# Kernel optimization log

Hardware: AMD Instinct MI355X
Metric: run time of the kernel (lower is better)

The kernel has to match this reference:

```python
import jax, jax.numpy as jnp
from jax import lax
import numpy as np

DN = ('NHWC', 'HWIO', 'NHWC')  # NHWC activations, HWIO kernels (TF layout)
EPS = 1e-3


def setup_inputs() -> dict:
    key = jax.random.key(0)
    ks = jax.random.split(key, 6)
    B, H, W, C = 16, 64, 64, 256
    x = jax.random.normal(ks[0], (B, H, W, C), jnp.float32)
    # per-sample predicted kernels (scaled to keep activations well-conditioned)
    depthwise_kernels = jax.random.normal(ks[1], (B, 3, 3, C, C), jnp.float32) * 0.02
    pointwise_kernels = jax.random.normal(ks[2], (B, 1, 1, C, C), jnp.float32) * 0.06
    biases = jax.random.normal(ks[3], (B, C), jnp.float32) * 0.1
    # shared trailing Conv2D layer params
    conv_w = jax.random.normal(ks[4], (3, 3, C, C), jnp.float32) * 0.02
    conv_b = jnp.zeros((C,), jnp.float32)
    return dict(x=x, depthwise_kernels=depthwise_kernels,
                pointwise_kernels=pointwise_kernels, biases=biases,
                conv_w=conv_w, conv_b=conv_b)


def _instance_norm(x):
    # tf.nn.moments over spatial dims (population variance), eps=0.001
    mean = jnp.mean(x, axis=(1, 2), keepdims=True)
    var = jnp.var(x, axis=(1, 2), keepdims=True)
    return (x - mean) * lax.rsqrt(var + EPS)


def _reflect_pad_hw(x, p=1):
    pad = [(0, 0)] * (x.ndim - 3) + [(p, p), (p, p), (0, 0)]
    return jnp.pad(x, pad, mode='reflect')


def _per_sample_conv(xi, dk, pk, bi):
    # xi: [H,W,C]; dk: [3,3,C,Cm]; pk: [1,1,Cm,Co]; bi: [Co]
    xp = _reflect_pad_hw(xi)[None]  # [1,H+2,W+2,C]
    y = lax.conv_general_dilated(xp, dk, (1, 1), 'VALID', dimension_numbers=DN)
    y = lax.conv_general_dilated(y, pk, (1, 1), 'VALID', dimension_numbers=DN)
    return (y + bi)[0]


def reference(x, depthwise_kernels, pointwise_kernels, biases, conv_w, conv_b):
    x = _instance_norm(x)
    # per-sample kernels -> vmap over batch (replaces tf.map_fn)
    x = jax.vmap(_per_sample_conv)(x, depthwise_kernels, pointwise_kernels, biases)
    # shared Conv2D: reflect pad + VALID conv + bias
    xp = _reflect_pad_hw(x)
    y = lax.conv_general_dilated(xp, conv_w, (1, 1), 'VALID', dimension_numbers=DN)
    return y + conv_b
```

## Files before the change

### kernel.cpp

```cpp
#include <hip/hip_runtime.h>


typedef __bf16 bf16x8 __attribute__((ext_vector_type(8)));
typedef float f32x4 __attribute__((ext_vector_type(4)));

__device__ __forceinline__ float bf2f(unsigned short v) {
    return __uint_as_float(((unsigned int)v) << 16);
}
__device__ __forceinline__ unsigned short f2bf(float f) {
    unsigned int u = __float_as_uint(f);
    unsigned int r = (u + 0x7FFFu + ((u >> 16) & 1u)) >> 16;
    return (unsigned short)r;
}
__device__ __forceinline__ float ldg_elem(const void* p, size_t idx, bool isbf) {
    return isbf ? bf2f(((const unsigned short*)p)[idx]) : ((const float*)p)[idx];
}

__device__ __forceinline__ void gload16(const void* g, void* l) {
    __builtin_amdgcn_global_load_lds(
        (__attribute__((address_space(1))) void*)(unsigned long long)g,
        (__attribute__((address_space(3))) void*)(unsigned long long)l,
        16, 0, 0);
}

#define RAW_BARRIER() do { asm volatile("" ::: "memory"); \
                           __builtin_amdgcn_s_barrier();   \
                           asm volatile("" ::: "memory"); } while (0)

__global__ void detect_dtype(const unsigned short* __restrict__ x, int* __restrict__ flag) {
    __shared__ int wild;
    if (threadIdx.x == 0) wild = 0;
    __syncthreads();
    int cnt = 0;
    for (int i = 0; i < 16; ++i) {
        float a = fabsf(bf2f(x[threadIdx.x * 16 + i]));
        if (!(a < 64.f) || (a != 0.f && a < 1e-5f)) cnt++;
    }
    atomicAdd(&wild, cnt);
    __syncthreads();
    if (threadIdx.x == 0) *flag = (wild > 512) ? 0 : 1;
}


__global__ void init_stats(float* s) { s[blockIdx.x * 256 + threadIdx.x] = 0.f; }

__global__ void norm_partial(const void* __restrict__ x, const int* __restrict__ flag,
                             float* __restrict__ ssum, float* __restrict__ ssq) {
    const bool isbf = (*flag != 0);
    const int b = blockIdx.x, chunk = blockIdx.y, c = threadIdx.x;
    const size_t base = ((size_t)(b * 4096 + chunk * 64)) * 256 + c;
    float s = 0.f, q = 0.f;
    for (int i = 0; i < 64; ++i) {
        float v = ldg_elem(x, base + (size_t)i * 256, isbf);
        s += v; q += v * v;
    }
    atomicAdd(&ssum[b * 256 + c], s);
    atomicAdd(&ssq[b * 256 + c], q);
}

__global__ void norm_finalize(float* ssum, float* ssq) {
    int i = blockIdx.x * 256 + threadIdx.x;
    float mean = ssum[i] * (1.f / 4096.f);
    float var  = ssq[i]  * (1.f / 4096.f) - mean * mean;
    ssum[i] = mean;
    ssq[i]  = rsqrtf(var + 1e-3f);
}

__global__ void norm_apply(const void* __restrict__ x, const int* __restrict__ flag,
                           const float* __restrict__ mean, const float* __restrict__ rstd,
                           unsigned short* __restrict__ xn) {
    const bool isbf = (*flag != 0);
    size_t e = ((size_t)blockIdx.x * 256 + threadIdx.x) * 8;
    int c0 = (int)(e & 255);
    int bc = (int)(e >> 20) * 256 + c0;
    float v[8];
    if (isbf) {
        uint4 raw = *(const uint4*)((const unsigned short*)x + e);
        unsigned int rr[4] = {raw.x, raw.y, raw.z, raw.w};
#pragma unroll
        for (int i = 0; i < 4; ++i) {
            v[2 * i]     = bf2f((unsigned short)(rr[i] & 0xFFFF));
            v[2 * i + 1] = bf2f((unsigned short)(rr[i] >> 16));
        }
    } else {
        float4 f0 = *(const float4*)((const float*)x + e);
        float4 f1 = *(const float4*)((const float*)x + e + 4);
        v[0] = f0.x; v[1] = f0.y; v[2] = f0.z; v[3] = f0.w;
        v[4] = f1.x; v[5] = f1.y; v[6] = f1.z; v[7] = f1.w;
    }
    unsigned int o[4];
#pragma unroll
    for (int i = 0; i < 4; ++i) {
        unsigned short lo = f2bf((v[2 * i]     - mean[bc + 2 * i])     * rstd[bc + 2 * i]);
        unsigned short hi = f2bf((v[2 * i + 1] - mean[bc + 2 * i + 1]) * rstd[bc + 2 * i + 1]);
        o[i] = (unsigned int)lo | ((unsigned int)hi << 16);
    }
    uint4 out; out.x = o[0]; out.y = o[1]; out.z = o[2]; out.w = o[3];
    *(uint4*)(xn + e) = out;
}

template <bool SCALE>
__global__ void transpose_wk(const void* __restrict__ src, const int* __restrict__ flag,
                             unsigned short* __restrict__ dst,
                             int s_per, long dstBStride, int coStride,
                             const float* __restrict__ rstd) {
    __shared__ unsigned short tile[64][66];
    const bool isbf = (*flag != 0);
    const int sl = blockIdx.x;
    const int b = sl / s_per;
    const size_t dbase = (size_t)b * (size_t)dstBStride + (size_t)(sl % s_per) * 256;
    const int ci0 = blockIdx.y * 64, co0 = blockIdx.z * 64;
    const int t = threadIdx.x;
    const int co4 = (t & 15) * 4;
    const int r0 = t >> 4;
#pragma unroll
    for (int i = 0; i < 4; ++i) {
        int r = r0 + i * 16;
        size_t sidx = (size_t)sl * 65536 + (size_t)(ci0 + r) * 256 + co0 + co4;
        if (isbf) {
            ushort4 v = *(const ushort4*)((const unsigned short*)src + sidx);
            tile[r][co4] = v.x; tile[r][co4 + 1] = v.y;
            tile[r][co4 + 2] = v.z; tile[r][co4 + 3] = v.w;
        } else {
            float4 v = *(const float4*)((const float*)src + sidx);
            tile[r][co4] = f2bf(v.x); tile[r][co4 + 1] = f2bf(v.y);
            tile[r][co4 + 2] = f2bf(v.z); tile[r][co4 + 3] = f2bf(v.w);
        }
    }
    __syncthreads();
    const int cip = (t & 31) * 2;
    const int cob = t >> 5;
    float s0 = 1.f, s1 = 1.f;
    if (SCALE) { s0 = rstd[b * 256 + ci0 + cip]; s1 = rstd[b * 256 + ci0 + cip + 1]; }
#pragma unroll
    for (int i = 0; i < 8; ++i) {
        int co = cob + i * 8;
        unsigned short lo = tile[cip][co], hi = tile[cip + 1][co];
        if (SCALE) { lo = f2bf(bf2f(lo) * s0); hi = f2bf(bf2f(hi) * s1); }
        *(unsigned int*)(dst + dbase + (size_t)(co0 + co) * coStride + ci0 + cip) =
            (unsigned int)lo | ((unsigned int)hi << 16);
    }
}

__global__ void corr_kernel(const unsigned short* __restrict__ dkT,
                            const float* __restrict__ mean,
                            float* __restrict__ negcorr) {
    const int b = blockIdx.x;
    const int lane = threadIdx.x & 63;
    const int co = blockIdx.y * 4 + (threadIdx.x >> 6);
    const unsigned short* wp = dkT + (size_t)(b * 256 + co) * 2304;
    const float* mb = mean + b * 256;
    const int ci0 = (lane & 31) * 8;
    float4 ma = *(const float4*)(mb + ci0);
    float4 mc = *(const float4*)(mb + ci0 + 4);
    float mm[8] = {ma.x, ma.y, ma.z, ma.w, mc.x, mc.y, mc.z, mc.w};
    float sum = 0.f;
#pragma unroll
    for (int c = 0; c < 5; ++c) {
        int k = c * 512 + lane * 8;
        if (k < 2304) {
            uint4 w = *(const uint4*)(wp + k);
            unsigned int wsv[4] = {w.x, w.y, w.z, w.w};
#pragma unroll
            for (int j = 0; j < 4; ++j) {
                sum += bf2f((unsigned short)(wsv[j] & 0xFFFF)) * mm[2 * j];
                sum += bf2f((unsigned short)(wsv[j] >> 16)) * mm[2 * j + 1];
            }
        }
    }
#pragma unroll
    for (int off = 32; off > 0; off >>= 1) sum += __shfl_down(sum, off);
    if (lane == 0) negcorr[b * 256 + co] = -sum;
}

template <int KSLICES, bool PER_SAMPLE_W, int BIAS_MODE, bool IS3X3, bool OUT_F32>
__global__ __launch_bounds__(512, 2) void gemm_conv_256(const unsigned short* __restrict__ src,
                                                        const int* __restrict__ flag,
                                                        const unsigned short* __restrict__ wT,
                                                        const void* __restrict__ bias,
                                                        void* __restrict__ dst) {
    constexpr int KTOT = KSLICES * 256;
    constexpr int NKT = KTOT / 64;
    static_assert(NKT >= 2, "pipeline needs >=2 K-tiles");
    extern __shared__ unsigned short smem[];

    const int t = threadIdx.x;
    const int lane = t & 63;
    const int wave = t >> 6;
    const int wr = wave >> 2;
    const int wc = wave & 3;
    const int b = blockIdx.z;
    const int m0 = blockIdx.x * 256;
    const unsigned short* srcB = src + (size_t)b * (4096 * 256);
    const unsigned short* wB = wT + (PER_SAMPLE_W ? (size_t)b * 256 * KTOT : (size_t)0);
    const bool in_bf = (BIAS_MODE >= 2) ? (*flag != 0) : true;

    const int trow = t >> 3;
    const int tswz = ((t & 7) ^ (trow & 7)) << 3;
    int hU[4], wU[4];
#pragma unroll
    for (int u = 0; u < 4; ++u) {
        int m = m0 + u * 64 + trow;
        hU[u] = m >> 6; wU[u] = m & 63;
    }
    const unsigned short* gBu[4];
#pragma unroll
    for (int u = 0; u < 4; ++u)
        gBu[u] = wB + (size_t)(u * 64 + trow) * KTOT + tswz;

    f32x4 acc[8][4];
#pragma unroll
    for (int i = 0; i < 8; ++i)
#pragma unroll
        for (int j = 0; j < 4; ++j) acc[i][j] = (f32x4){0.f, 0.f, 0.f, 0.f};

    const int fr = lane & 15;
    const int quad = lane >> 4;
    const int fsw = fr & 7;
    const int ks0 = ((quad) ^ fsw) << 3;
    const int ks1 = ((quad + 4) ^ fsw) << 3;
    const int rm = wr * 128;
    const int cn = wc * 64;

#pragma unroll
    for (int kt = 0; kt < 2; ++kt) {
        const int s0_ = kt >> 2;
        const int pdh = IS3X3 ? (s0_ / 3) - 1 : 0;
        const int pdw = IS3X3 ? (s0_ % 3) - 1 : 0;
        const int pchb = (kt & 3) << 6;
        unsigned short* ldsAW = smem + kt * 32768 + wave * 512;
#pragma unroll
        for (int u = 0; u < 4; ++u) {
            int hh = hU[u] + pdh; hh = (hh < 0) ? 1 : (hh > 63 ? 62 : hh);
            int ww = wU[u] + pdw; ww = (ww < 0) ? 1 : (ww > 63 ? 62 : ww);
            gload16(srcB + (size_t)((hh << 6) + ww) * 256 + pchb + tswz, ldsAW + u * 4096);
        }
#pragma unroll
        for (int u = 0; u < 4; ++u)
            gload16(gBu[u] + (size_t)kt * 64, ldsAW + 16384 + u * 4096);
    }
    asm volatile("s_waitcnt vmcnt(8)" ::: "memory");
    RAW_BARRIER();

    bf16x8 af[4][2], bfr[4][2];

    for (int i = 0; i < NKT; ++i) {
        const int buf = i & 1;
        const unsigned short* As_b = smem + buf * 32768;
        const unsigned short* Bs_b = As_b + 16384;
        unsigned short* ldsAW = smem + buf * 32768 + wave * 512;
        const int kt2 = i + 2;
        const bool st = (kt2 < NKT);
        int dh2 = 0, dw2 = 0, chb2 = 0;
        if (st) {
            int s2 = kt2 >> 2;
            dh2 = IS3X3 ? (s2 / 3) - 1 : 0;
            dw2 = IS3X3 ? (s2 % 3) - 1 : 0;
            chb2 = (kt2 & 3) << 6;
        }

#pragma unroll
        for (int m = 0; m < 4; ++m) {
            const unsigned short* rp = As_b + (rm + m * 16 + fr) * 64;
            af[m][0] = *(const bf16x8*)(rp + ks0);
            af[m][1] = *(const bf16x8*)(rp + ks1);
        }
#pragma unroll
        for (int n = 0; n < 2; ++n) {
            const unsigned short* rp = Bs_b + (cn + n * 16 + fr) * 64;
            bfr[n][0] = *(const bf16x8*)(rp + ks0);
            bfr[n][1] = *(const bf16x8*)(rp + ks1);
        }
        __builtin_amdgcn_s_setprio(1);
#pragma unroll
        for (int m = 0; m < 4; ++m)
#pragma unroll
            for (int n = 0; n < 2; ++n) {
                acc[m][n] = __builtin_amdgcn_mfma_f32_16x16x32_bf16(af[m][0], bfr[n][0], acc[m][n], 0, 0, 0);
                acc[m][n] = __builtin_amdgcn_mfma_f32_16x16x32_bf16(af[m][1], bfr[n][1], acc[m][n], 0, 0, 0);
            }
        __builtin_amdgcn_s_setprio(0);

#pragma unroll
        for (int n = 2; n < 4; ++n) {
            const unsigned short* rp = Bs_b + (cn + n * 16 + fr) * 64;
            bfr[n][0] = *(const bf16x8*)(rp + ks0);
            bfr[n][1] = *(const bf16x8*)(rp + ks1);
        }
        __builtin_amdgcn_s_setprio(1);
#pragma unroll
        for (int m = 0; m < 4; ++m)
#pragma unroll
            for (int n = 2; n < 4; ++n) {
                acc[m][n] = __builtin_amdgcn_mfma_f32_16x16x32_bf16(af[m][0], bfr[n][0], acc[m][n], 0, 0, 0);
                acc[m][n] = __builtin_amdgcn_mfma_f32_16x16x32_bf16(af[m][1], bfr[n][1], acc[m][n], 0, 0, 0);
            }
        __builtin_amdgcn_s_setprio(0);

#pragma unroll
        for (int m = 0; m < 4; ++m) {
            const unsigned short* rp = As_b + (rm + 64 + m * 16 + fr) * 64;
            af[m][0] = *(const bf16x8*)(rp + ks0);
            af[m][1] = *(const bf16x8*)(rp + ks1);
        }
        __builtin_amdgcn_s_setprio(1);
#pragma unroll
        for (int m = 0; m < 4; ++m)
#pragma unroll
            for (int n = 0; n < 4; ++n) {
                acc[4 + m][n] = __builtin_amdgcn_mfma_f32_16x16x32_bf16(af[m][0], bfr[n][0], acc[4 + m][n], 0, 0, 0);
                acc[4 + m][n] = __builtin_amdgcn_mfma_f32_16x16x32_bf16(af[m][1], bfr[n][1], acc[4 + m][n], 0, 0, 0);
            }
        __builtin_amdgcn_s_setprio(0);

        RAW_BARRIER();
        if (st) {
#pragma unroll
            for (int u = 0; u < 4; ++u) {
                int hh = hU[u] + dh2; hh = (hh < 0) ? 1 : (hh > 63 ? 62 : hh);
                int ww = wU[u] + dw2; ww = (ww < 0) ? 1 : (ww > 63 ? 62 : ww);
                gload16(srcB + (size_t)((hh << 6) + ww) * 256 + chb2 + tswz, ldsAW + u * 4096);
            }
#pragma unroll
            for (int u = 0; u < 4; ++u)
                gload16(gBu[u] + (size_t)kt2 * 64, ldsAW + 16384 + u * 4096);
            asm volatile("s_waitcnt vmcnt(8)" ::: "memory");
        } else if (i + 1 < NKT) {
            asm volatile("s_waitcnt vmcnt(0)" ::: "memory");
        }
        RAW_BARRIER();
    }

    const int rbase = quad * 4;
    float bv[4];
#pragma unroll
    for (int n = 0; n < 4; ++n) {
        int nn = cn + n * 16 + fr;
        if (BIAS_MODE == 2)      bv[n] = ldg_elem(bias, b * 256 + nn, in_bf);
        else if (BIAS_MODE == 3) bv[n] = ldg_elem(bias, nn, in_bf);
        else                     bv[n] = 0.f;
    }
#pragma unroll
    for (int m = 0; m < 8; ++m) {
#pragma unroll
        for (int rr = 0; rr < 4; ++rr) {
            int mm = m0 + rm + m * 16 + rbase + rr;
            size_t rowoff = ((size_t)b * 4096 + mm) * 256;
#pragma unroll
            for (int n = 0; n < 4; ++n) {
                int nn = cn + n * 16 + fr;
                float val = acc[m][n][rr] + bv[n];
                if (OUT_F32) ((float*)dst)[rowoff + nn] = val;
                else         ((unsigned short*)dst)[rowoff + nn] = f2bf(val);
            }
        }
    }
}

template <int KSLICES, bool PER_SAMPLE_W, int BIAS_MODE, bool IS3X3, bool OUT_F32>
__global__ __launch_bounds__(256) void gemm_conv_dma(const unsigned short* __restrict__ src,
                                                     const int* __restrict__ flag,
                                                     const unsigned short* __restrict__ wT,
                                                     const void* __restrict__ bias,
                                                     void* __restrict__ dst) {
    constexpr int KTOT = KSLICES * 256;
    __shared__ unsigned short As[128 * 64];
    __shared__ unsigned short Bs[128 * 64];

    const int t = threadIdx.x;
    const int lane = t & 63;
    const int wave = t >> 6;
    const int b = blockIdx.z;
    const int m0 = blockIdx.x * 128;
    const int n0 = blockIdx.y * 128;
    const unsigned short* srcB = src + (size_t)b * (4096 * 256);
    const unsigned short* wB = wT + (PER_SAMPLE_W ? (size_t)b * 256 * KTOT : (size_t)0);
    const bool in_bf = (BIAS_MODE >= 2) ? (*flag != 0) : true;

    f32x4 acc[4][4];
#pragma unroll
    for (int i = 0; i < 4; ++i)
#pragma unroll
        for (int j = 0; j < 4; ++j) acc[i][j] = (f32x4){0.f, 0.f, 0.f, 0.f};

    const int lr = lane >> 3;
    const int cidx = lane & 7;
    const int swz = ((cidx ^ lr) << 3);

    int hA[4], wA[4];
    const unsigned short* gB[4];
    unsigned short* ldsA[4];
    unsigned short* ldsB[4];
#pragma unroll
    for (int c = 0; c < 4; ++c) {
        int r = wave * 32 + c * 8;
        int m = m0 + r + lr;
        hA[c] = m >> 6; wA[c] = m & 63;
        gB[c] = wB + (size_t)(n0 + r + lr) * KTOT + swz;
        ldsA[c] = As + r * 64;
        ldsB[c] = Bs + r * 64;
    }

    const int fr = lane & 15;
    const int quad = lane >> 4;
    const int rm = (wave >> 1) * 64;
    const int cn = (wave & 1) * 64;
    const int fsw = fr & 7;

    for (int s = 0; s < KSLICES; ++s) {
        const int dh = IS3X3 ? (s / 3) - 1 : 0;
        const int dw = IS3X3 ? (s % 3) - 1 : 0;
        const unsigned short* gA[4];
#pragma unroll
        for (int c = 0; c < 4; ++c) {
            int hh = hA[c] + dh; hh = (hh < 0) ? 1 : (hh > 63 ? 62 : hh);
            int ww = wA[c] + dw; ww = (ww < 0) ? 1 : (ww > 63 ? 62 : ww);
            gA[c] = srcB + (size_t)((hh << 6) + ww) * 256 + swz;
        }
        const int kbase = s * 256;
#pragma unroll
        for (int cc = 0; cc < 4; ++cc) {
            __syncthreads();
#pragma unroll
            for (int c = 0; c < 4; ++c) {
                gload16(gA[c] + cc * 64, ldsA[c]);
                gload16(gB[c] + kbase + cc * 64, ldsB[c]);
            }
            __syncthreads();

#pragma unroll
            for (int step = 0; step < 2; ++step) {
                const int ks = ((quad + step * 4) ^ fsw) << 3;
                bf16x8 af[4], bfr[4];
#pragma unroll
                for (int i = 0; i < 4; ++i)
                    af[i] = *(const bf16x8*)&As[(rm + i * 16 + fr) * 64 + ks];
#pragma unroll
                for (int j = 0; j < 4; ++j)
                    bfr[j] = *(const bf16x8*)&Bs[(cn + j * 16 + fr) * 64 + ks];
#pragma unroll
                for (int i = 0; i < 4; ++i)
#pragma unroll
                    for (int j = 0; j < 4; ++j)
                        acc[i][j] = __builtin_amdgcn_mfma_f32_16x16x32_bf16(af[i], bfr[j], acc[i][j], 0, 0, 0);
            }
        }
    }

    const int rbase = quad * 4;
    const int col = fr;
    float bv[4];
#pragma unroll
    for (int j = 0; j < 4; ++j) {
        int n = n0 + cn + j * 16 + col;
        if (BIAS_MODE == 2)      bv[j] = ldg_elem(bias, b * 256 + n, in_bf);
        else if (BIAS_MODE == 3) bv[j] = ldg_elem(bias, n, in_bf);
        else                     bv[j] = 0.f;
    }
#pragma unroll
    for (int i = 0; i < 4; ++i) {
#pragma unroll
        for (int rr = 0; rr < 4; ++rr) {
            int m = m0 + rm + i * 16 + rbase + rr;
            size_t rowoff = ((size_t)b * 4096 + m) * 256;
#pragma unroll
            for (int j = 0; j < 4; ++j) {
                int n = n0 + cn + j * 16 + col;
                float val = acc[i][j][rr] + bv[j];
                if (OUT_F32) ((float*)dst)[rowoff + n] = val;
                else         ((unsigned short*)dst)[rowoff + n] = f2bf(val);
            }
        }
    }
}

template <int KSLICES, bool PER_SAMPLE_W, int BIAS_MODE, bool IS3X3, bool SRC_ADAPT, bool OUT_F32>
__global__ __launch_bounds__(256) void gemm_conv(const void* __restrict__ src,
                                                 const int* __restrict__ flag,
                                                 const unsigned short* __restrict__ wT,
                                                 const void* __restrict__ bias,
                                                 void* __restrict__ dst) {
    constexpr int KTOT = KSLICES * 256;
    __shared__ unsigned short As[128][40];
    __shared__ unsigned short Bs[128][40];

    const bool in_bf = (SRC_ADAPT || BIAS_MODE >= 2) ? (*flag != 0) : true;
    const int t = threadIdx.x;
    const int b = blockIdx.z;
    const int m0 = blockIdx.x * 128;
    const int n0 = blockIdx.y * 128;
    const size_t srcOfs = (size_t)b * (4096 * 256);
    const unsigned short* wB = wT + (PER_SAMPLE_W ? (size_t)b * 256 * KTOT : (size_t)0);

    f32x4 acc[4][4];
#pragma unroll
    for (int i = 0; i < 4; ++i)
#pragma unroll
        for (int j = 0; j < 4; ++j) acc[i][j] = (f32x4){0.f, 0.f, 0.f, 0.f};

    const int lane = t & 63;
    const int wave = t >> 6;
    const int rm = (wave >> 1) * 64;
    const int cn = (wave & 1) * 64;
    const int fr = lane & 15;
    const int kg = (lane >> 4) * 8;

    for (int kk = 0; kk < KTOT / 32; ++kk) {
        const int k0 = kk * 32;
        const int s = k0 >> 8;
        const int ci0 = k0 & 255;
        const int dh = IS3X3 ? (s / 3) - 1 : 0;
        const int dw = IS3X3 ? (s % 3) - 1 : 0;
        __syncthreads();
#pragma unroll
        for (int cc = 0; cc < 2; ++cc) {
            int ch = t + cc * 256;
            int r = ch >> 2;
            int ko = (ch & 3) << 3;
            int m = m0 + r;
            int h = m >> 6, w = m & 63;
            if (IS3X3) {
                h += dh; h = (h < 0) ? 1 : (h > 63 ? 62 : h);
                w += dw; w = (w < 0) ? 1 : (w > 63 ? 62 : w);
            }
            size_t eidx = srcOfs + (size_t)((h << 6) + w) * 256 + ci0 + ko;
            if (!SRC_ADAPT || in_bf) {
                uint4 v = *(const uint4*)((const unsigned short*)src + eidx);
                *(uint4*)&As[r][ko] = v;
            } else {
                const float* sf = (const float*)src + eidx;
                float4 f0 = *(const float4*)sf;
                float4 f1 = *(const float4*)(sf + 4);
                uint4 v;
                v.x = (unsigned int)f2bf(f0.x) | ((unsigned int)f2bf(f0.y) << 16);
                v.y = (unsigned int)f2bf(f0.z) | ((unsigned int)f2bf(f0.w) << 16);
                v.z = (unsigned int)f2bf(f1.x) | ((unsigned int)f2bf(f1.y) << 16);
                v.w = (unsigned int)f2bf(f1.z) | ((unsigned int)f2bf(f1.w) << 16);
                *(uint4*)&As[r][ko] = v;
            }
        }
#pragma unroll
        for (int cc = 0; cc < 2; ++cc) {
            int ch = t + cc * 256;
            int n = ch >> 2;
            int ko = (ch & 3) << 3;
            uint4 v = *(const uint4*)(wB + (size_t)(n0 + n) * KTOT + k0 + ko);
            *(uint4*)&Bs[n][ko] = v;
        }
        __syncthreads();

        bf16x8 af[4], bfr[4];
#pragma unroll
        for (int i = 0; i < 4; ++i) af[i] = *(const bf16x8*)&As[rm + i * 16 + fr][kg];
#pragma unroll
        for (int j = 0; j < 4; ++j) bfr[j] = *(const bf16x8*)&Bs[cn + j * 16 + fr][kg];
#pragma unroll
        for (int i = 0; i < 4; ++i)
#pragma unroll
            for (int j = 0; j < 4; ++j)
                acc[i][j] = __builtin_amdgcn_mfma_f32_16x16x32_bf16(af[i], bfr[j], acc[i][j], 0, 0, 0);
    }

    const int rbase = (lane >> 4) * 4;
    const int col = lane & 15;
    float bv[4];
#pragma unroll
    for (int j = 0; j < 4; ++j) {
        int n = n0 + cn + j * 16 + col;
        if (BIAS_MODE == 1)      bv[j] = ((const float*)bias)[b * 256 + n];
        else if (BIAS_MODE == 2) bv[j] = ldg_elem(bias, b * 256 + n, in_bf);
        else if (BIAS_MODE == 3) bv[j] = ldg_elem(bias, n, in_bf);
        else                     bv[j] = 0.f;
    }
#pragma unroll
    for (int i = 0; i < 4; ++i) {
#pragma unroll
        for (int rr = 0; rr < 4; ++rr) {
            int m = m0 + rm + i * 16 + rbase + rr;
            size_t rowoff = ((size_t)b * 4096 + m) * 256;
#pragma unroll
            for (int j = 0; j < 4; ++j) {
                int n = n0 + cn + j * 16 + col;
                float val = acc[i][j][rr] + bv[j];
                if (OUT_F32) ((float*)dst)[rowoff + n] = val;
                else         ((unsigned short*)dst)[rowoff + n] = f2bf(val);
            }
        }
    }
}

extern "C" void kernel_launch(void* const* d_in, const int* in_sizes, int n_in,
                              void* d_out, int out_size, void* d_ws, size_t ws_size,
                              hipStream_t stream) {
    const void* x    = d_in[0];
    const void* dk   = d_in[1];
    const void* pk   = d_in[2];
    const void* bias = d_in[3];
    const void* cw   = d_in[4];
    const void* cb   = d_in[5];

    const size_t NEED_SMALL = 36896768u;
    const size_t NEED_BIG   = 55771136u;
    if (ws_size < NEED_SMALL) return;
    const bool big = (ws_size >= NEED_BIG);

    char* ws = (char*)d_ws;
    int*   flagp   = (int*)ws;
    float* meanp   = (float*)(ws + 1024);
    float* rstdp   = (float*)(ws + 17408);
    float* negcorr = (float*)(ws + 33792);
    unsigned short* pkT = (unsigned short*)(ws + 65536);
    unsigned short* cwT = (unsigned short*)(ws + 2162688);
    unsigned short* dkT = (unsigned short*)(ws + 3342336);
    unsigned short* xn  = (unsigned short*)(ws + 22216704);
    unsigned short* y2  = big ? xn : dkT;
    unsigned short* y1  = (unsigned short*)d_out;

    hipFuncSetAttribute(reinterpret_cast<const void*>(gemm_conv_256<9, true, 0, true, false>),
                        hipFuncAttributeMaxDynamicSharedMemorySize, 131072);
    hipFuncSetAttribute(reinterpret_cast<const void*>(gemm_conv_256<9, false, 3, true, true>),
                        hipFuncAttributeMaxDynamicSharedMemorySize, 131072);

    detect_dtype<<<1, 256, 0, stream>>>((const unsigned short*)x, flagp);
    init_stats<<<32, 256, 0, stream>>>(meanp);
    norm_partial<<<dim3(16, 64), 256, 0, stream>>>(x, flagp, meanp, rstdp);
    norm_finalize<<<16, 256, 0, stream>>>(meanp, rstdp);

    transpose_wk<false><<<dim3(16, 4, 4), 256, 0, stream>>>(pk, flagp, pkT, 1, 65536L, 256, nullptr);
    transpose_wk<false><<<dim3(9, 4, 4), 256, 0, stream>>>(cw, flagp, cwT, 9, 0L, 2304, nullptr);

    if (big) {
        transpose_wk<false><<<dim3(144, 4, 4), 256, 0, stream>>>(dk, flagp, dkT, 9, 589824L, 2304, nullptr);
        norm_apply<<<8192, 256, 0, stream>>>(x, flagp, meanp, rstdp, xn);
        gemm_conv_256<9, true, 0, true, false><<<dim3(16, 1, 16), 512, 131072, stream>>>(xn, flagp, dkT, nullptr, y1);
    } else {
        transpose_wk<true><<<dim3(144, 4, 4), 256, 0, stream>>>(dk, flagp, dkT, 9, 589824L, 2304, rstdp);
        corr_kernel<<<dim3(16, 64), 256, 0, stream>>>(dkT, meanp, negcorr);
        gemm_conv<9, true, 1, true, true, false><<<dim3(32, 2, 16), 256, 0, stream>>>(x, flagp, dkT, negcorr, y1);
    }

    gemm_conv_dma<1, true, 2, false, false><<<dim3(32, 2, 16), 256, 0, stream>>>(y1, flagp, pkT, bias, y2);
    gemm_conv_256<9, false, 3, true, true><<<dim3(16, 1, 16), 512, 131072, stream>>>(y2, flagp, cwT, cb, d_out);
}
```

Before: 378.7 us.

## Replace atomic norm stats, reuse pipelined GEMM for pointwise conv, remap blocks

Instance-norm statistics now come from vectorized per-chunk partial sums written to workspace and reduced in a finalize kernel, which removes the atomics and the init kernel. The 1x1 pointwise conv now runs on the double-buffered 256x256 gemm_conv_256 kernel instead of the older single-buffered DMA kernel. The block index is remapped so that consecutive blocks span different samples. A-tile gather offsets are cached per 3x3 tap rather than recomputed for every K-tile. The partial-sum buffers alias the xn workspace, and the pointwise GEMM now launches 256 large blocks rather than 1024 smaller ones.

```diff
diff --git a/kernel.cpp b/kernel.cpp
--- a/kernel.cpp
+++ b/kernel.cpp
@@ -41,29 +41,60 @@
     if (threadIdx.x == 0) *flag = (wild > 512) ? 0 : 1;
 }
 
-
-__global__ void init_stats(float* s) { s[blockIdx.x * 256 + threadIdx.x] = 0.f; }
-
-__global__ void norm_partial(const void* __restrict__ x, const int* __restrict__ flag,
-                             float* __restrict__ ssum, float* __restrict__ ssq) {
+__global__ void norm_partial2(const void* __restrict__ x, const int* __restrict__ flag,
+                              float* __restrict__ partS, float* __restrict__ partQ) {
     const bool isbf = (*flag != 0);
-    const int b = blockIdx.x, chunk = blockIdx.y, c = threadIdx.x;
-    const size_t base = ((size_t)(b * 4096 + chunk * 64)) * 256 + c;
+    const int b = blockIdx.x, ch = blockIdx.y;
+    const int t = threadIdx.x;
+    const int l = t & 63;
+    const int c4 = l * 4;
+    const int sp0 = t >> 6;
+    const size_t base = ((size_t)(b * 4096 + ch * 128 + sp0)) * 256 + c4;
+    float s[4] = {0.f, 0.f, 0.f, 0.f}, q[4] = {0.f, 0.f, 0.f, 0.f};
+    if (isbf) {
+        for (int i = 0; i < 32; ++i) {
+            const unsigned short* p = (const unsigned short*)x + base + (size_t)i * 1024;
+            ushort4 v = *(const ushort4*)p;
+            float a[4] = {bf2f(v.x), bf2f(v.y), bf2f(v.z), bf2f(v.w)};
+#pragma unroll
+            for (int j = 0; j < 4; ++j) { s[j] += a[j]; q[j] += a[j] * a[j]; }
+        }
+    } else {
+        for (int i = 0; i < 32; ++i) {
+            float4 v = *(const float4*)((const float*)x + base + (size_t)i * 1024);
+            float a[4] = {v.x, v.y, v.z, v.w};
+#pragma unroll
+            for (int j = 0; j < 4; ++j) { s[j] += a[j]; q[j] += a[j] * a[j]; }
+        }
+    }
+    __shared__ float red[4][64][9];
+#pragma unroll
+    for (int j = 0; j < 4; ++j) { red[sp0][l][j] = s[j]; red[sp0][l][4 + j] = q[j]; }
+    __syncthreads();
+    if (t < 64) {
+#pragma unroll
+        for (int j = 0; j < 4; ++j) {
+            float ss = red[0][t][j] + red[1][t][j] + red[2][t][j] + red[3][t][j];
+            float qq = red[0][t][4 + j] + red[1][t][4 + j] + red[2][t][4 + j] + red[3][t][4 + j];
+            int c = t * 4 + j;
+            partS[(b * 32 + ch) * 256 + c] = ss;
+            partQ[(b * 32 + ch) * 256 + c] = qq;
+        }
+    }
+}
+
+__global__ void norm_finalize2(const float* __restrict__ partS, const float* __restrict__ partQ,
+                               float* __restrict__ mean, float* __restrict__ rstd) {
+    const int b = blockIdx.x, c = threadIdx.x;
     float s = 0.f, q = 0.f;
-    for (int i = 0; i < 64; ++i) {
-        float v = ldg_elem(x, base + (size_t)i * 256, isbf);
-        s += v; q += v * v;
-    }
-    atomicAdd(&ssum[b * 256 + c], s);
-    atomicAdd(&ssq[b * 256 + c], q);
-}
-
-__global__ void norm_finalize(float* ssum, float* ssq) {
-    int i = blockIdx.x * 256 + threadIdx.x;
-    float mean = ssum[i] * (1.f / 4096.f);
-    float var  = ssq[i]  * (1.f / 4096.f) - mean * mean;
-    ssum[i] = mean;
-    ssq[i]  = rsqrtf(var + 1e-3f);
+    for (int k = 0; k < 32; ++k) {
+        s += partS[(b * 32 + k) * 256 + c];
+        q += partQ[(b * 32 + k) * 256 + c];
+    }
+    float m = s * (1.f / 4096.f);
+    float v = q * (1.f / 4096.f) - m * m;
+    mean[b * 256 + c] = m;
+    rstd[b * 256 + c] = rsqrtf(v + 1e-3f);
 }
 
 __global__ void norm_apply(const void* __restrict__ x, const int* __restrict__ flag,
@@ -189,8 +220,9 @@
     const int wave = t >> 6;
     const int wr = wave >> 2;
     const int wc = wave & 3;
-    const int b = blockIdx.z;
-    const int m0 = blockIdx.x * 256;
+    const int bid = blockIdx.x + 16 * blockIdx.z;
+    const int b  = (bid & 7) + ((bid >> 3) & 1) * 8;
+    const int m0 = (bid >> 4) * 256;
     const unsigned short* srcB = src + (size_t)b * (4096 * 256);
     const unsigned short* wB = wT + (PER_SAMPLE_W ? (size_t)b * 256 * KTOT : (size_t)0);
     const bool in_bf = (BIAS_MODE >= 2) ? (*flag != 0) : true;
@@ -224,9 +256,8 @@
 
 #pragma unroll
     for (int kt = 0; kt < 2; ++kt) {
-        const int s0_ = kt >> 2;
-        const int pdh = IS3X3 ? (s0_ / 3) - 1 : 0;
-        const int pdw = IS3X3 ? (s0_ % 3) - 1 : 0;
+        const int pdh = IS3X3 ? -1 : 0;
+        const int pdw = IS3X3 ? -1 : 0;
         const int pchb = (kt & 3) << 6;
         unsigned short* ldsAW = smem + kt * 32768 + wave * 512;
 #pragma unroll
@@ -243,6 +274,8 @@
     RAW_BARRIER();
 
     bf16x8 af[4][2], bfr[4][2];
+    size_t aoff[4];
+    int cur_s = -1;
 
     for (int i = 0; i < NKT; ++i) {
         const int buf = i & 1;
@@ -251,13 +284,6 @@
         unsigned short* ldsAW = smem + buf * 32768 + wave * 512;
         const int kt2 = i + 2;
         const bool st = (kt2 < NKT);
-        int dh2 = 0, dw2 = 0, chb2 = 0;
-        if (st) {
-            int s2 = kt2 >> 2;
-            dh2 = IS3X3 ? (s2 / 3) - 1 : 0;
-            dw2 = IS3X3 ? (s2 % 3) - 1 : 0;
-            chb2 = (kt2 & 3) << 6;
-        }
 
 #pragma unroll
         for (int m = 0; m < 4; ++m) {
@@ -315,12 +341,28 @@
 
         RAW_BARRIER();
         if (st) {
-#pragma unroll
-            for (int u = 0; u < 4; ++u) {
-                int hh = hU[u] + dh2; hh = (hh < 0) ? 1 : (hh > 63 ? 62 : hh);
-                int ww = wU[u] + dw2; ww = (ww < 0) ? 1 : (ww > 63 ? 62 : ww);
-                gload16(srcB + (size_t)((hh << 6) + ww) * 256 + chb2 + tswz, ldsAW + u * 4096);
-            }
+            if (IS3X3) {
+                const int s2 = kt2 >> 2;
+                if (s2 != cur_s) {
+                    cur_s = s2;
+                    const int dh2 = s2 / 3 - 1, dw2 = s2 % 3 - 1;
+#pragma unroll
+                    for (int u = 0; u < 4; ++u) {
+                        int hh = hU[u] + dh2; hh = (hh < 0) ? 1 : (hh > 63 ? 62 : hh);
+                        int ww = wU[u] + dw2; ww = (ww < 0) ? 1 : (ww > 63 ? 62 : ww);
+                        aoff[u] = (size_t)((hh << 6) + ww) * 256 + tswz;
+                    }
+                }
+            } else if (cur_s < 0) {
+                cur_s = 0;
+#pragma unroll
+                for (int u = 0; u < 4; ++u)
+                    aoff[u] = (size_t)((hU[u] << 6) + wU[u]) * 256 + tswz;
+            }
+            const int chb2 = (kt2 & 3) << 6;
+#pragma unroll
+            for (int u = 0; u < 4; ++u)
+                gload16(srcB + aoff[u] + chb2, ldsAW + u * 4096);
 #pragma unroll
             for (int u = 0; u < 4; ++u)
                 gload16(gBu[u] + (size_t)kt2 * 64, ldsAW + 16384 + u * 4096);
@@ -352,123 +394,6 @@
                 float val = acc[m][n][rr] + bv[n];
                 if (OUT_F32) ((float*)dst)[rowoff + nn] = val;
                 else         ((unsigned short*)dst)[rowoff + nn] = f2bf(val);
-            }
-        }
-    }
-}
-
-template <int KSLICES, bool PER_SAMPLE_W, int BIAS_MODE, bool IS3X3, bool OUT_F32>
-__global__ __launch_bounds__(256) void gemm_conv_dma(const unsigned short* __restrict__ src,
-                                                     const int* __restrict__ flag,
-                                                     const unsigned short* __restrict__ wT,
-                                                     const void* __restrict__ bias,
-                                                     void* __restrict__ dst) {
-    constexpr int KTOT = KSLICES * 256;
-    __shared__ unsigned short As[128 * 64];
-    __shared__ unsigned short Bs[128 * 64];
-
-    const int t = threadIdx.x;
-    const int lane = t & 63;
-    const int wave = t >> 6;
-    const int b = blockIdx.z;
-    const int m0 = blockIdx.x * 128;
-    const int n0 = blockIdx.y * 128;
-    const unsigned short* srcB = src + (size_t)b * (4096 * 256);
-    const unsigned short* wB = wT + (PER_SAMPLE_W ? (size_t)b * 256 * KTOT : (size_t)0);
-    const bool in_bf = (BIAS_MODE >= 2) ? (*flag != 0) : true;
-
-    f32x4 acc[4][4];
-#pragma unroll
-    for (int i = 0; i < 4; ++i)
-#pragma unroll
-        for (int j = 0; j < 4; ++j) acc[i][j] = (f32x4){0.f, 0.f, 0.f, 0.f};
-
-    const int lr = lane >> 3;
-    const int cidx = lane & 7;
-    const int swz = ((cidx ^ lr) << 3);
-
-    int hA[4], wA[4];
-    const unsigned short* gB[4];
-    unsigned short* ldsA[4];
-    unsigned short* ldsB[4];
-#pragma unroll
-    for (int c = 0; c < 4; ++c) {
-        int r = wave * 32 + c * 8;
-        int m = m0 + r + lr;
-        hA[c] = m >> 6; wA[c] = m & 63;
-        gB[c] = wB + (size_t)(n0 + r + lr) * KTOT + swz;
-        ldsA[c] = As + r * 64;
-        ldsB[c] = Bs + r * 64;
-    }
-
-    const int fr = lane & 15;
-    const int quad = lane >> 4;
-    const int rm = (wave >> 1) * 64;
-    const int cn = (wave & 1) * 64;
-    const int fsw = fr & 7;
-
-    for (int s = 0; s < KSLICES; ++s) {
-        const int dh = IS3X3 ? (s / 3) - 1 : 0;
-        const int dw = IS3X3 ? (s % 3) - 1 : 0;
-        const unsigned short* gA[4];
-#pragma unroll
-        for (int c = 0; c < 4; ++c) {
-            int hh = hA[c] + dh; hh = (hh < 0) ? 1 : (hh > 63 ? 62 : hh);
-            int ww = wA[c] + dw; ww = (ww < 0) ? 1 : (ww > 63 ? 62 : ww);
-            gA[c] = srcB + (size_t)((hh << 6) + ww) * 256 + swz;
-        }
-        const int kbase = s * 256;
-#pragma unroll
-        for (int cc = 0; cc < 4; ++cc) {
-            __syncthreads();
-#pragma unroll
-            for (int c = 0; c < 4; ++c) {
-                gload16(gA[c] + cc * 64, ldsA[c]);
-                gload16(gB[c] + kbase + cc * 64, ldsB[c]);
-            }
-            __syncthreads();
-
-#pragma unroll
-            for (int step = 0; step < 2; ++step) {
-                const int ks = ((quad + step * 4) ^ fsw) << 3;
-                bf16x8 af[4], bfr[4];
-#pragma unroll
-                for (int i = 0; i < 4; ++i)
-                    af[i] = *(const bf16x8*)&As[(rm + i * 16 + fr) * 64 + ks];
-#pragma unroll
-                for (int j = 0; j < 4; ++j)
-                    bfr[j] = *(const bf16x8*)&Bs[(cn + j * 16 + fr) * 64 + ks];
-#pragma unroll
-                for (int i = 0; i < 4; ++i)
-#pragma unroll
-                    for (int j = 0; j < 4; ++j)
-                        acc[i][j] = __builtin_amdgcn_mfma_f32_16x16x32_bf16(af[i], bfr[j], acc[i][j], 0, 0, 0);
-            }
-        }
-    }
-
-    const int rbase = quad * 4;
-    const int col = fr;
-    float bv[4];
-#pragma unroll
-    for (int j = 0; j < 4; ++j) {
-        int n = n0 + cn + j * 16 + col;
-        if (BIAS_MODE == 2)      bv[j] = ldg_elem(bias, b * 256 + n, in_bf);
-        else if (BIAS_MODE == 3) bv[j] = ldg_elem(bias, n, in_bf);
-        else                     bv[j] = 0.f;
-    }
-#pragma unroll
-    for (int i = 0; i < 4; ++i) {
-#pragma unroll
-        for (int rr = 0; rr < 4; ++rr) {
-            int m = m0 + rm + i * 16 + rbase + rr;
-            size_t rowoff = ((size_t)b * 4096 + m) * 256;
-#pragma unroll
-            for (int j = 0; j < 4; ++j) {
-                int n = n0 + cn + j * 16 + col;
-                float val = acc[i][j][rr] + bv[j];
-                if (OUT_F32) ((float*)dst)[rowoff + n] = val;
-                else         ((unsigned short*)dst)[rowoff + n] = f2bf(val);
             }
         }
     }
@@ -613,18 +538,21 @@
     unsigned short* cwT = (unsigned short*)(ws + 2162688);
     unsigned short* dkT = (unsigned short*)(ws + 3342336);
     unsigned short* xn  = (unsigned short*)(ws + 22216704);
+    float* partS = (float*)(ws + 22216704);
+    float* partQ = (float*)(ws + 22216704 + 524288);
     unsigned short* y2  = big ? xn : dkT;
     unsigned short* y1  = (unsigned short*)d_out;
 
     hipFuncSetAttribute(reinterpret_cast<const void*>(gemm_conv_256<9, true, 0, true, false>),
+                        hipFuncAttributeMaxDynamicSharedMemorySize, 131072);
+    hipFuncSetAttribute(reinterpret_cast<const void*>(gemm_conv_256<1, true, 2, false, false>),
                         hipFuncAttributeMaxDynamicSharedMemorySize, 131072);
     hipFuncSetAttribute(reinterpret_cast<const void*>(gemm_conv_256<9, false, 3, true, true>),
                         hipFuncAttributeMaxDynamicSharedMemorySize, 131072);
 
     detect_dtype<<<1, 256, 0, stream>>>((const unsigned short*)x, flagp);
-    init_stats<<<32, 256, 0, stream>>>(meanp);
-    norm_partial<<<dim3(16, 64), 256, 0, stream>>>(x, flagp, meanp, rstdp);
-    norm_finalize<<<16, 256, 0, stream>>>(meanp, rstdp);
+    norm_partial2<<<dim3(16, 32), 256, 0, stream>>>(x, flagp, partS, partQ);
+    norm_finalize2<<<16, 256, 0, stream>>>(partS, partQ, meanp, rstdp);
 
     transpose_wk<false><<<dim3(16, 4, 4), 256, 0, stream>>>(pk, flagp, pkT, 1, 65536L, 256, nullptr);
     transpose_wk<false><<<dim3(9, 4, 4), 256, 0, stream>>>(cw, flagp, cwT, 9, 0L, 2304, nullptr);
@@ -639,6 +567,6 @@
         gemm_conv<9, true, 1, true, true, false><<<dim3(32, 2, 16), 256, 0, stream>>>(x, flagp, dkT, negcorr, y1);
     }
 
-    gemm_conv_dma<1, true, 2, false, false><<<dim3(32, 2, 16), 256, 0, stream>>>(y1, flagp, pkT, bias, y2);
+    gemm_conv_256<1, true, 2, false, false><<<dim3(16, 1, 16), 512, 131072, stream>>>(y1, flagp, pkT, bias, y2);
     gemm_conv_256<9, false, 3, true, true><<<dim3(16, 1, 16), 512, 131072, stream>>>(y2, flagp, cwT, cb, d_out);
 }
```

New measurement: 352.5 us. -6.9%, faster.
